# Kernel tuning notes

Measured on AMD Instinct MI355X. Metric: run time of the kernel, lower is better.

## Reference

```python
import jax, jax.numpy as jnp
import numpy as np

B, S, C = 2, 2048, 512
E, H = 512, 8
HD = E // H
SCALE = HD ** -0.5


def setup_inputs() -> dict:
    key = jax.random.key(0)
    ks = jax.random.split(key, 10)
    s = 1.0 / np.sqrt(C)
    return {
        "x": jax.random.normal(ks[0], (B, S, C), dtype=jnp.float32),
        "dist_map": jax.random.uniform(ks[1], (B, H, S, S), dtype=jnp.float32),
        "mask": jax.random.randint(ks[2], (B, S), 0, 2, dtype=jnp.int32),
        "Wq": jax.random.normal(ks[3], (E, C), dtype=jnp.float32) * s,
        "bq": jnp.zeros((E,), dtype=jnp.float32),
        "Wk": jax.random.normal(ks[4], (E, C), dtype=jnp.float32) * s,
        "bk": jnp.zeros((E,), dtype=jnp.float32),
        "Wv": jax.random.normal(ks[5], (E, C), dtype=jnp.float32) * s,
        "bv": jnp.zeros((E,), dtype=jnp.float32),
        "Wo": jax.random.normal(ks[6], (E, E), dtype=jnp.float32) * (1.0 / np.sqrt(E)),
        "bo": jnp.zeros((E,), dtype=jnp.float32),
    }


def reference(x, dist_map, mask, Wq, bq, Wk, bk, Wv, bv, Wo, bo):
    # NOTE: faithful to original torch code: .view(B, H, S, HD) without transpose
    q = (x @ Wq.T + bq).reshape(B, H, S, HD)
    k = (x @ Wk.T + bk).reshape(B, H, S, HD)
    v = (x @ Wv.T + bv).reshape(B, H, S, HD)
    attn = jnp.einsum('bhqd,bhkd->bhqk', q, k)
    pad = mask.astype(bool)[:, None, None, :]  # [B,1,1,S]
    attn = jnp.where(pad, jnp.float32(-10000.0), attn)
    attn = jax.nn.softmax(attn * SCALE, axis=-1)
    attn = (attn + dist_map) * 0.5  # post-softmax dist_map blend
    # dropout p=0.0 -> identity
    attn_probs = attn
    ctx = jnp.einsum('bhal,bhlv->bhav', attn_probs, v)  # [B,H,S,HD]
    ctx = ctx.transpose(0, 2, 1, 3).reshape(B, S, E)
    out = ctx @ Wo.T + bo
    return (out, attn_probs)
```

## Files before the change

### kernel.cpp

```cpp
#include <hip/hip_runtime.h>
#include <stdint.h>

typedef __attribute__((ext_vector_type(4))) float  f32x4;
typedef __attribute__((ext_vector_type(8))) short  short8;
typedef __attribute__((ext_vector_type(4))) short  short4v;

#define MFMA16(a,b,c) __builtin_amdgcn_mfma_f32_16x16x32_bf16((a),(b),(c),0,0,0)

static __device__ __forceinline__ unsigned short f2bf(float f) {
    unsigned int u = __float_as_uint(f);
    u += 0x7FFFu + ((u >> 16) & 1u);
    return (unsigned short)(u >> 16);
}
static __device__ __forceinline__ float bflo(unsigned int v) {
    return __uint_as_float(v << 16);
}
static __device__ __forceinline__ float bfhi(unsigned int v) {
    return __uint_as_float(v & 0xFFFF0000u);
}
static __device__ __forceinline__ float bf2f(unsigned short v) {
    return __uint_as_float(((unsigned int)v) << 16);
}
static __device__ __forceinline__ unsigned int packbf(float a, float b) {
    return (unsigned int)f2bf(a) | ((unsigned int)f2bf(b) << 16);
}


__global__ __launch_bounds__(256) void qkv_gemm(
    const float* __restrict__ x,
    const float* __restrict__ Wq, const float* __restrict__ bq,
    const float* __restrict__ Wk, const float* __restrict__ bk,
    const float* __restrict__ Wv, const float* __restrict__ bv,
    unsigned short* __restrict__ Qb, unsigned short* __restrict__ Kb,
    unsigned short* __restrict__ Vb)
{
    __shared__ unsigned short As[128 * 40];
    __shared__ unsigned short Bs[128 * 40];

    const int tid  = threadIdx.x;
    const int lane = tid & 63;
    const int wid  = tid >> 6;
    const int g = lane >> 4, c = lane & 15;
    const int wr = wid >> 1, wc = wid & 1;
    const int bm    = blockIdx.x;
    const int widx  = blockIdx.y >> 2;
    const int ntile = blockIdx.y & 3;

    const float* W    = (widx == 0) ? Wq : (widx == 1) ? Wk : Wv;
    const float* bias = (widx == 0) ? bq : (widx == 1) ? bk : bv;
    unsigned short* Y = (widx == 0) ? Qb : (widx == 1) ? Kb : Vb;
    const float* Abase = x + (size_t)bm * 128 * 512;
    const float* Bbase = W + (size_t)ntile * 128 * 512;

    f32x4 acc[4][4];
    #pragma unroll
    for (int m = 0; m < 4; m++)
        #pragma unroll
        for (int n = 0; n < 4; n++) acc[m][n] = (f32x4){0.f, 0.f, 0.f, 0.f};

    for (int kk = 0; kk < 512; kk += 32) {
        #pragma unroll
        for (int i = 0; i < 4; i++) {
            int f  = i * 256 + tid;
            int rr = f >> 3;
            int cc = (f & 7) * 4;
            f32x4 va = *(const f32x4*)(Abase + rr * 512 + kk + cc);
            f32x4 vb = *(const f32x4*)(Bbase + rr * 512 + kk + cc);
            short4v sa, sb;
            #pragma unroll
            for (int q = 0; q < 4; q++) { sa[q] = (short)f2bf(va[q]); sb[q] = (short)f2bf(vb[q]); }
            *(short4v*)(&As[rr * 40 + cc]) = sa;
            *(short4v*)(&Bs[rr * 40 + cc]) = sb;
        }
        __syncthreads();

        short8 af[4], bfr[4];
        #pragma unroll
        for (int m = 0; m < 4; m++) af[m]  = *(const short8*)(&As[(wr * 64 + m * 16 + c) * 40 + g * 8]);
        #pragma unroll
        for (int n = 0; n < 4; n++) bfr[n] = *(const short8*)(&Bs[(wc * 64 + n * 16 + c) * 40 + g * 8]);
        #pragma unroll
        for (int m = 0; m < 4; m++)
            #pragma unroll
            for (int n = 0; n < 4; n++)
                acc[m][n] = MFMA16(af[m], bfr[n], acc[m][n]);
        __syncthreads();
    }

    #pragma unroll
    for (int n = 0; n < 4; n++) {
        int colW = ntile * 128 + wc * 64 + n * 16 + c;
        float bb = bias[colW];
        #pragma unroll
        for (int m = 0; m < 4; m++) {
            #pragma unroll
            for (int r = 0; r < 4; r++) {
                int row = bm * 128 + wr * 64 + m * 16 + g * 4 + r;
                Y[(size_t)row * 512 + colW] = f2bf(acc[m][n][r] + bb);
            }
        }
    }
}

__global__ __launch_bounds__(256) void v_transpose(
    const unsigned short* __restrict__ Vb, unsigned short* __restrict__ Vt)
{
    __shared__ unsigned short T[8][520];

    const int tid = threadIdx.x;
    const int t   = blockIdx.x;
    const int bh  = blockIdx.y;
    const int b = bh >> 3, h = bh & 7;

    #pragma unroll
    for (int i = 0; i < 2; i++) {
        int idx = i * 256 + tid;
        int j   = idx >> 6;
        int cc  = (idx & 63) * 8;
        short8 v = *(const short8*)(Vb + (size_t)(b * 2048 + h * 256 + t * 8 + j) * 512 + cc);
        *(short8*)(&T[j][cc]) = v;
    }
    __syncthreads();

    const int d   = tid >> 2;
    const int sjb = (tid & 3) * 16;
    unsigned short tmp[16];
    #pragma unroll
    for (int i = 0; i < 16; i++) {
        int sj = sjb + i;
        tmp[i] = T[sj >> 3][(sj & 7) * 64 + d];
    }
    unsigned short* dst = Vt + ((size_t)(bh * 64 + d) * 2048) + t * 64 + sjb;
    *(short8*)(dst)     = *(short8*)(&tmp[0]);
    *(short8*)(dst + 8) = *(short8*)(&tmp[8]);
}

__global__ __launch_bounds__(256) void attn_kernel(
    const unsigned short* __restrict__ Qb, const unsigned short* __restrict__ Kb,
    const unsigned short* __restrict__ Vt,
    const float* __restrict__ dist, const int* __restrict__ mask,
    float* __restrict__ attn_out, unsigned short* __restrict__ ctx_bf)
{
    __shared__ unsigned short AP[4][16][72];
    __shared__ float red[4][2][16];
    __shared__ float Cred[4][16][64];

    const int tid = threadIdx.x;
    const int lane = tid & 63, wid = tid >> 6;
    const int g = lane >> 4, c = lane & 15;

    const int wg  = blockIdx.x + gridDim.x * blockIdx.y;
    const int qg  = (wg >> 3) & 127;
    const int bh  = (wg & 7) * 2 + ((wg >> 10) & 1);
    const int b = bh >> 3, h = bh & 7;

    const unsigned short* Qh  = Qb + (size_t)b * 1048576 + (size_t)h * 131072;
    const unsigned short* Kh  = Kb + (size_t)b * 1048576 + (size_t)h * 131072;
    const unsigned short* Vth = Vt + (size_t)bh * 131072;
    const float* distb = dist + (size_t)bh * 4194304;
    float*       outb  = attn_out + (size_t)bh * 4194304;
    const int*   maskb = mask + b * 2048;

    const int qrow    = qg * 16;
    const int keybase = wid * 512;

    short8 qf[2];
    #pragma unroll
    for (int ks = 0; ks < 2; ks++)
        qf[ks] = *(const short8*)(Qh + (size_t)(qrow + c) * 64 + ks * 32 + g * 8);

    unsigned int pl[8][4][2];
    float lmax[4] = {-3e38f, -3e38f, -3e38f, -3e38f};

    #pragma unroll
    for (int kb8 = 0; kb8 < 8; kb8++) {
        const int kb = keybase + kb8 * 64;
        short8 kf[4][2];
        #pragma unroll
        for (int n = 0; n < 4; n++)
            #pragma unroll
            for (int ks = 0; ks < 2; ks++)
                kf[n][ks] = *(const short8*)(Kh + (size_t)(kb + n * 16 + c) * 64 + ks * 32 + g * 8);
        #pragma unroll
        for (int n = 0; n < 4; n++) {
            f32x4 z = (f32x4){0.f, 0.f, 0.f, 0.f};
            z = MFMA16(qf[0], kf[n][0], z);
            z = MFMA16(qf[1], kf[n][1], z);
            const int mv = maskb[kb + n * 16 + c];
            float l[4];
            #pragma unroll
            for (int r = 0; r < 4; r++) {
                l[r] = mv ? -1250.f : z[r] * 0.125f;
                lmax[r] = fmaxf(lmax[r], l[r]);
            }
            pl[kb8][n][0] = packbf(l[0], l[1]);
            pl[kb8][n][1] = packbf(l[2], l[3]);
        }
    }
    #pragma unroll
    for (int r = 0; r < 4; r++) {
        #pragma unroll
        for (int off = 1; off < 16; off <<= 1)
            lmax[r] = fmaxf(lmax[r], __shfl_xor(lmax[r], off));
    }
    if (c == 0) {
        #pragma unroll
        for (int r = 0; r < 4; r++) red[wid][0][g * 4 + r] = lmax[r];
    }
    __syncthreads();
    float m[4];
    #pragma unroll
    for (int r = 0; r < 4; r++) {
        int row = g * 4 + r;
        m[r] = fmaxf(fmaxf(red[0][0][row], red[1][0][row]),
                     fmaxf(red[2][0][row], red[3][0][row]));
    }

    float dsum[4] = {0.f, 0.f, 0.f, 0.f};
    #pragma unroll
    for (int kb8 = 0; kb8 < 8; kb8++) {
        #pragma unroll
        for (int n = 0; n < 4; n++) {
            #pragma unroll
            for (int pi = 0; pi < 2; pi++) {
                unsigned int v = pl[kb8][n][pi];
                float e0 = __expf(bflo(v) - m[pi * 2]);
                float e1 = __expf(bfhi(v) - m[pi * 2 + 1]);
                dsum[pi * 2]     += e0;
                dsum[pi * 2 + 1] += e1;
                pl[kb8][n][pi] = packbf(e0, e1);
            }
        }
    }
    #pragma unroll
    for (int r = 0; r < 4; r++) {
        #pragma unroll
        for (int off = 1; off < 16; off <<= 1)
            dsum[r] += __shfl_xor(dsum[r], off);
    }
    if (c == 0) {
        #pragma unroll
        for (int r = 0; r < 4; r++) red[wid][1][g * 4 + r] = dsum[r];
    }
    __syncthreads();
    float invd[4];
    #pragma unroll
    for (int r = 0; r < 4; r++) {
        int row = g * 4 + r;
        invd[r] = 1.f / (red[0][1][row] + red[1][1][row] + red[2][1][row] + red[3][1][row]);
    }

    f32x4 cacc[4];
    #pragma unroll
    for (int nd = 0; nd < 4; nd++) cacc[nd] = (f32x4){0.f, 0.f, 0.f, 0.f};

    #pragma unroll
    for (int kb8 = 0; kb8 < 8; kb8++) {
        const int kb = keybase + kb8 * 64;

        f32x4 dv[4];
        #pragma unroll
        for (int rg = 0; rg < 4; rg++)
            dv[rg] = *(const f32x4*)(distb + (size_t)(qrow + rg * 4 + g) * 2048 + kb + c * 4);

        #pragma unroll
        for (int n = 0; n < 4; n++) {
            #pragma unroll
            for (int pi = 0; pi < 2; pi++) {
                unsigned int v = pl[kb8][n][pi];
                AP[wid][g * 4 + pi * 2    ][n * 16 + c] = f2bf(bflo(v) * invd[pi * 2]);
                AP[wid][g * 4 + pi * 2 + 1][n * 16 + c] = f2bf(bfhi(v) * invd[pi * 2 + 1]);
            }
        }

        #pragma unroll
        for (int rg = 0; rg < 4; rg++) {
            const int row = rg * 4 + g;
            short4v pv = *(const short4v*)(&AP[wid][row][c * 4]);
            f32x4 apv;
            #pragma unroll
            for (int q = 0; q < 4; q++)
                apv[q] = 0.5f * (bf2f((unsigned short)pv[q]) + dv[rg][q]);
            *(f32x4*)(outb + (size_t)(qrow + row) * 2048 + kb + c * 4) = apv;
            short4v apb;
            #pragma unroll
            for (int q = 0; q < 4; q++) apb[q] = (short)f2bf(apv[q]);
            *(short4v*)(&AP[wid][row][c * 4]) = apb;
        }

        short8 apf[2];
        #pragma unroll
        for (int ks = 0; ks < 2; ks++)
            apf[ks] = *(const short8*)(&AP[wid][c][ks * 32 + g * 8]);
        #pragma unroll
        for (int nd = 0; nd < 4; nd++) {
            #pragma unroll
            for (int ks = 0; ks < 2; ks++) {
                short8 vf = *(const short8*)(Vth + (size_t)(nd * 16 + c) * 2048 + kb + ks * 32 + g * 8);
                cacc[nd] = MFMA16(apf[ks], vf, cacc[nd]);
            }
        }
    }

    #pragma unroll
    for (int nd = 0; nd < 4; nd++)
        #pragma unroll
        for (int r = 0; r < 4; r++)
            Cred[wid][g * 4 + r][nd * 16 + c] = cacc[nd][r];
    __syncthreads();

    for (int e = tid; e < 1024; e += 256) {
        int row = e >> 6, d = e & 63;
        float s = Cred[0][row][d] + Cred[1][row][d] + Cred[2][row][d] + Cred[3][row][d];
        int i = qrow + row;
        ctx_bf[(size_t)(b * 2048 + i) * 512 + h * 64 + d] = f2bf(s);
    }
}

__global__ __launch_bounds__(256) void out_gemm(
    const unsigned short* __restrict__ A,
    const float* __restrict__ Wo, const float* __restrict__ bo,
    float* __restrict__ out)
{
    __shared__ unsigned short As[128 * 40];
    __shared__ unsigned short Bs[128 * 40];

    const int tid  = threadIdx.x;
    const int lane = tid & 63;
    const int wid  = tid >> 6;
    const int g = lane >> 4, c = lane & 15;
    const int wr = wid >> 1, wc = wid & 1;
    const int bm    = blockIdx.x;
    const int ntile = blockIdx.y;

    const unsigned short* Abase = A + (size_t)bm * 128 * 512;
    const float* Bbase = Wo + (size_t)ntile * 128 * 512;

    f32x4 acc[4][4];
    #pragma unroll
    for (int m = 0; m < 4; m++)
        #pragma unroll
        for (int n = 0; n < 4; n++) acc[m][n] = (f32x4){0.f, 0.f, 0.f, 0.f};

    for (int kk = 0; kk < 512; kk += 32) {
        #pragma unroll
        for (int i = 0; i < 2; i++) {
            int f8 = i * 256 + tid;
            int rr = f8 >> 2;
            int cc = (f8 & 3) * 8;
            short8 va = *(const short8*)(Abase + (size_t)rr * 512 + kk + cc);
            *(short8*)(&As[rr * 40 + cc]) = va;
        }
        #pragma unroll
        for (int i = 0; i < 4; i++) {
            int f  = i * 256 + tid;
            int rr = f >> 3;
            int cc = (f & 7) * 4;
            f32x4 vb = *(const f32x4*)(Bbase + (size_t)rr * 512 + kk + cc);
            short4v sb;
            #pragma unroll
            for (int q = 0; q < 4; q++) sb[q] = (short)f2bf(vb[q]);
            *(short4v*)(&Bs[rr * 40 + cc]) = sb;
        }
        __syncthreads();

        short8 af[4], bfr[4];
        #pragma unroll
        for (int m = 0; m < 4; m++) af[m]  = *(const short8*)(&As[(wr * 64 + m * 16 + c) * 40 + g * 8]);
        #pragma unroll
        for (int n = 0; n < 4; n++) bfr[n] = *(const short8*)(&Bs[(wc * 64 + n * 16 + c) * 40 + g * 8]);
        #pragma unroll
        for (int m = 0; m < 4; m++)
            #pragma unroll
            for (int n = 0; n < 4; n++)
                acc[m][n] = MFMA16(af[m], bfr[n], acc[m][n]);
        __syncthreads();
    }

    #pragma unroll
    for (int n = 0; n < 4; n++) {
        int col = ntile * 128 + wc * 64 + n * 16 + c;
        float bb = bo[col];
        #pragma unroll
        for (int m = 0; m < 4; m++) {
            #pragma unroll
            for (int r = 0; r < 4; r++) {
                int row = bm * 128 + wr * 64 + m * 16 + g * 4 + r;
                out[(size_t)row * 512 + col] = acc[m][n][r] + bb;
            }
        }
    }
}

extern "C" void kernel_launch(void* const* d_in, const int* in_sizes, int n_in,
                              void* d_out, int out_size, void* d_ws, size_t ws_size,
                              hipStream_t stream)
{
    const float* x    = (const float*)d_in[0];
    const float* dist = (const float*)d_in[1];
    const int*   mask = (const int*)d_in[2];
    const float* Wq   = (const float*)d_in[3];
    const float* bq   = (const float*)d_in[4];
    const float* Wk   = (const float*)d_in[5];
    const float* bk   = (const float*)d_in[6];
    const float* Wv   = (const float*)d_in[7];
    const float* bv   = (const float*)d_in[8];
    const float* Wo   = (const float*)d_in[9];
    const float* bo   = (const float*)d_in[10];

    float* out      = (float*)d_out;
    float* attn_out = out + 2097152;

    char* ws = (char*)d_ws;
    unsigned short* Qb  = (unsigned short*)(ws);
    unsigned short* Kb  = (unsigned short*)(ws + (4u << 20));
    unsigned short* Vb  = (unsigned short*)(ws + (8u << 20));
    unsigned short* Vt  = (unsigned short*)(ws + (12u << 20));
    unsigned short* ctx = (unsigned short*)(ws + (8u << 20));

    qkv_gemm   <<<dim3(32, 12), 256, 0, stream>>>(x, Wq, bq, Wk, bk, Wv, bv, Qb, Kb, Vb);
    v_transpose<<<dim3(32, 16), 256, 0, stream>>>(Vb, Vt);
    attn_kernel<<<dim3(128, 16), 256, 0, stream>>>(Qb, Kb, Vt, dist, mask, attn_out, ctx);
    out_gemm   <<<dim3(32, 4),  256, 0, stream>>>(ctx, Wo, bo, out);
}
```

Measured before the change: 245.6 us.

## Double-buffer dist_map tiles into LDS via async global_load_lds in attention

Streams the dist_map tiles through a per-wave double buffer in shared memory using global_load_lds, so the next tile's loads are in flight while the current tile is processed. A block-wide barrier is added on every iteration. Softmax now uses exp2f with log2e folded into the scale and mask constants, and the final cross-wave ctx reduction uses vectorized 16-byte LDS reads with padded rows and 8-byte stores. Shared memory use rises to 32KB for the staging buffer, which is reused for the reduction, and this may lower occupancy.

```diff
diff --git a/kernel.cpp b/kernel.cpp
--- a/kernel.cpp
+++ b/kernel.cpp
@@ -6,21 +6,19 @@
 typedef __attribute__((ext_vector_type(4))) short  short4v;
 
 #define MFMA16(a,b,c) __builtin_amdgcn_mfma_f32_16x16x32_bf16((a),(b),(c),0,0,0)
+
+typedef __attribute__((address_space(1))) void gv_t;
+typedef __attribute__((address_space(3))) void lv_t;
+#define GLL16(g,l) __builtin_amdgcn_global_load_lds((const gv_t*)(g), (lv_t*)(l), 16, 0, 0)
 
 static __device__ __forceinline__ unsigned short f2bf(float f) {
     unsigned int u = __float_as_uint(f);
     u += 0x7FFFu + ((u >> 16) & 1u);
     return (unsigned short)(u >> 16);
 }
-static __device__ __forceinline__ float bflo(unsigned int v) {
-    return __uint_as_float(v << 16);
-}
-static __device__ __forceinline__ float bfhi(unsigned int v) {
-    return __uint_as_float(v & 0xFFFF0000u);
-}
-static __device__ __forceinline__ float bf2f(unsigned short v) {
-    return __uint_as_float(((unsigned int)v) << 16);
-}
+static __device__ __forceinline__ float bflo(unsigned int v) { return __uint_as_float(v << 16); }
+static __device__ __forceinline__ float bfhi(unsigned int v) { return __uint_as_float(v & 0xFFFF0000u); }
+static __device__ __forceinline__ float bf2f(unsigned short v) { return __uint_as_float(((unsigned int)v) << 16); }
 static __device__ __forceinline__ unsigned int packbf(float a, float b) {
     return (unsigned int)f2bf(a) | ((unsigned int)f2bf(b) << 16);
 }
@@ -143,7 +141,7 @@
 {
     __shared__ unsigned short AP[4][16][72];
     __shared__ float red[4][2][16];
-    __shared__ float Cred[4][16][64];
+    __shared__ __attribute__((aligned(16))) float UN[8192];
 
     const int tid = threadIdx.x;
     const int lane = tid & 63, wid = tid >> 6;
@@ -164,6 +162,9 @@
     const int qrow    = qg * 16;
     const int keybase = wid * 512;
 
+    const float SC      = 0.18033688011f;
+    const float MASKVAL = -1803.3688f;
+
     short8 qf[2];
     #pragma unroll
     for (int ks = 0; ks < 2; ks++)
@@ -190,7 +191,7 @@
             float l[4];
             #pragma unroll
             for (int r = 0; r < 4; r++) {
-                l[r] = mv ? -1250.f : z[r] * 0.125f;
+                l[r] = mv ? MASKVAL : z[r] * SC;
                 lmax[r] = fmaxf(lmax[r], l[r]);
             }
             pl[kb8][n][0] = packbf(l[0], l[1]);
@@ -224,8 +225,8 @@
             #pragma unroll
             for (int pi = 0; pi < 2; pi++) {
                 unsigned int v = pl[kb8][n][pi];
-                float e0 = __expf(bflo(v) - m[pi * 2]);
-                float e1 = __expf(bfhi(v) - m[pi * 2 + 1]);
+                float e0 = exp2f(bflo(v) - m[pi * 2]);
+                float e1 = exp2f(bfhi(v) - m[pi * 2 + 1]);
                 dsum[pi * 2]     += e0;
                 dsum[pi * 2 + 1] += e1;
                 pl[kb8][n][pi] = packbf(e0, e1);
@@ -254,20 +255,33 @@
     #pragma unroll
     for (int nd = 0; nd < 4; nd++) cacc[nd] = (f32x4){0.f, 0.f, 0.f, 0.f};
 
-    #pragma unroll
-    for (int kb8 = 0; kb8 < 8; kb8++) {
-        const int kb = keybase + kb8 * 64;
-
-        f32x4 dv[4];
-        #pragma unroll
-        for (int rg = 0; rg < 4; rg++)
-            dv[rg] = *(const f32x4*)(distb + (size_t)(qrow + rg * 4 + g) * 2048 + kb + c * 4);
+    const float* dsrc = distb + (size_t)(qrow + (lane >> 4)) * 2048 + keybase + (lane & 15) * 4;
+    float* stg0 = &UN[wid * 2048];
+    float* stg1 = stg0 + 1024;
+
+    #pragma unroll
+    for (int ch = 0; ch < 4; ch++)
+        GLL16(dsrc + ch * 4 * 2048, stg0 + ch * 256);
+    __syncthreads();
+
+    #pragma unroll
+    for (int t = 0; t < 8; t++) {
+        const int kb = keybase + t * 64;
+        float* cur = (t & 1) ? stg1 : stg0;
+        float* nxt = (t & 1) ? stg0 : stg1;
+
+        if (t < 7) {
+            const float* ns = dsrc + (t + 1) * 64;
+            #pragma unroll
+            for (int ch = 0; ch < 4; ch++)
+                GLL16(ns + ch * 4 * 2048, nxt + ch * 256);
+        }
 
         #pragma unroll
         for (int n = 0; n < 4; n++) {
             #pragma unroll
             for (int pi = 0; pi < 2; pi++) {
-                unsigned int v = pl[kb8][n][pi];
+                unsigned int v = pl[t][n][pi];
                 AP[wid][g * 4 + pi * 2    ][n * 16 + c] = f2bf(bflo(v) * invd[pi * 2]);
                 AP[wid][g * 4 + pi * 2 + 1][n * 16 + c] = f2bf(bfhi(v) * invd[pi * 2 + 1]);
             }
@@ -276,11 +290,12 @@
         #pragma unroll
         for (int rg = 0; rg < 4; rg++) {
             const int row = rg * 4 + g;
+            f32x4 dvv = *(const f32x4*)(cur + row * 64 + c * 4);
             short4v pv = *(const short4v*)(&AP[wid][row][c * 4]);
             f32x4 apv;
             #pragma unroll
             for (int q = 0; q < 4; q++)
-                apv[q] = 0.5f * (bf2f((unsigned short)pv[q]) + dv[rg][q]);
+                apv[q] = 0.5f * (bf2f((unsigned short)pv[q]) + dvv[q]);
             *(f32x4*)(outb + (size_t)(qrow + row) * 2048 + kb + c * 4) = apv;
             short4v apb;
             #pragma unroll
@@ -300,8 +315,11 @@
                 cacc[nd] = MFMA16(apf[ks], vf, cacc[nd]);
             }
         }
-    }
-
+
+        __syncthreads();
+    }
+
+    float (*Cred)[16][68] = (float (*)[16][68])UN;
     #pragma unroll
     for (int nd = 0; nd < 4; nd++)
         #pragma unroll
@@ -309,11 +327,20 @@
             Cred[wid][g * 4 + r][nd * 16 + c] = cacc[nd][r];
     __syncthreads();
 
-    for (int e = tid; e < 1024; e += 256) {
-        int row = e >> 6, d = e & 63;
-        float s = Cred[0][row][d] + Cred[1][row][d] + Cred[2][row][d] + Cred[3][row][d];
-        int i = qrow + row;
-        ctx_bf[(size_t)(b * 2048 + i) * 512 + h * 64 + d] = f2bf(s);
+    {
+        const int q  = tid >> 4;
+        const int dq = (tid & 15) * 4;
+        f32x4 s = *(const f32x4*)(&Cred[0][q][dq]);
+        #pragma unroll
+        for (int w = 1; w < 4; w++) {
+            f32x4 t2 = *(const f32x4*)(&Cred[w][q][dq]);
+            #pragma unroll
+            for (int j = 0; j < 4; j++) s[j] += t2[j];
+        }
+        short4v cb;
+        #pragma unroll
+        for (int j = 0; j < 4; j++) cb[j] = (short)f2bf(s[j]);
+        *(short4v*)(ctx_bf + (size_t)(b * 2048 + qrow + q) * 512 + h * 64 + dq) = cb;
     }
 }
 
```

Result: slower. 262.9 us (+7.0%).
